# Kernel optimization log

Hardware: AMD Instinct MI355X
Metric: run time of the kernel (lower is better)

The kernel has to match this reference:

```python
import jax, jax.numpy as jnp
import numpy as np

IN_C = 256
KEY_C = 256
VAL_C = 256
HEADS = 8


def setup_inputs() -> dict:
    key = jax.random.key(0)
    ks = jax.random.split(key, 9)
    s = 0.02
    return {
        "x": jax.random.normal(ks[0], (4, 8192, IN_C), dtype=jnp.float32),
        "Wk": jax.random.normal(ks[1], (KEY_C, IN_C), dtype=jnp.float32) * s,
        "bk": jax.random.normal(ks[2], (KEY_C,), dtype=jnp.float32) * s,
        "Wq": jax.random.normal(ks[3], (KEY_C, IN_C), dtype=jnp.float32) * s,
        "bq": jax.random.normal(ks[4], (KEY_C,), dtype=jnp.float32) * s,
        "Wv": jax.random.normal(ks[5], (VAL_C, IN_C), dtype=jnp.float32) * s,
        "bv": jax.random.normal(ks[6], (VAL_C,), dtype=jnp.float32) * s,
        "Wr": jax.random.normal(ks[7], (IN_C, VAL_C), dtype=jnp.float32) * s,
        "br": jax.random.normal(ks[8], (IN_C,), dtype=jnp.float32) * s,
    }


def reference(x, Wk, bk, Wq, bq, Wv, bv, Wr, br):
    n, N, c = x.shape
    # Faithful to torch: reshape (NOT transpose) of (n, N, c) into (n, c, N)
    xi = x.reshape(n, c, N)
    # 1x1 convs == channel-mixing matmuls over the token axis
    K = jnp.einsum('oc,ncs->nos', Wk, xi) + bk[None, :, None]
    Q = jnp.einsum('oc,ncs->nos', Wq, xi) + bq[None, :, None]
    V = jnp.einsum('oc,ncs->nos', Wv, xi) + bv[None, :, None]
    dk = KEY_C // HEADS
    dv = VAL_C // HEADS
    Kh = K.reshape(n, HEADS, dk, N)
    Qh = Q.reshape(n, HEADS, dk, N)
    Vh = V.reshape(n, HEADS, dv, N)
    # keys: softmax over tokens (dim=2); queries: softmax over head key channels (dim=1)
    Kh = jax.nn.softmax(Kh, axis=3)
    Qh = jax.nn.softmax(Qh, axis=2)
    # context = K @ V^T : [n, H, dk, dv]
    ctx = jnp.einsum('nhks,nhvs->nhkv', Kh, Vh)
    # attended = context^T @ Q : [n, H, dv, N]
    att = jnp.einsum('nhkv,nhks->nhvs', ctx, Qh)
    agg = att.reshape(n, VAL_C, N)
    rep = jnp.einsum('ov,nvs->nos', Wr, agg) + br[None, :, None]
    out = rep + xi  # residual in (n, c, N) layout
    return jnp.transpose(out, (0, 2, 1))  # (n, N, c)
```

## Files before the change

### kernel.cpp

```cpp
#include <hip/hip_runtime.h>
#include <hip/hip_bf16.h>

#define NTOK 8192
#define NCH  256
#define TT   128
#define XTP  264
#define EK2  136

typedef unsigned short u16;
typedef __attribute__((ext_vector_type(8))) short bf16x8;
typedef __attribute__((ext_vector_type(4))) float f32x4;
typedef __attribute__((ext_vector_type(8))) unsigned short u16x8;
typedef __attribute__((ext_vector_type(4))) unsigned short u16x4;

__device__ __forceinline__ float b2f(u16 v){
  union { u16 u; __hip_bfloat16 h; } c; c.u = v; return __bfloat162float(c.h);
}
__device__ __forceinline__ u16 f2b(float f){
  union { __hip_bfloat16 h; u16 u; } c; c.h = __float2bfloat16(f); return c.u;
}
__device__ __forceinline__ f32x4 mfma16(bf16x8 a, bf16x8 b, f32x4 c){
  return __builtin_amdgcn_mfma_f32_16x16x32_bf16(a, b, c, 0, 0, 0);
}

__device__ __forceinline__ void stage_xtile(const float* __restrict__ xb,
                                            u16* scratch, u16* dst, int t)
{
  #pragma unroll
  for (int i = 0; i < 8; ++i) {
    int ch = i * 32 + (t >> 4);
    int tk = (t & 15) * 8;
    const float* p = xb + (size_t)ch * NTOK + tk;
    float4 v0 = *(const float4*)p;
    float4 v1 = *(const float4*)(p + 4);
    u16x8 pk;
    pk[0]=f2b(v0.x); pk[1]=f2b(v0.y); pk[2]=f2b(v0.z); pk[3]=f2b(v0.w);
    pk[4]=f2b(v1.x); pk[5]=f2b(v1.y); pk[6]=f2b(v1.z); pk[7]=f2b(v1.w);
    *(u16x8*)&scratch[ch * EK2 + tk] = pk;
  }
  __syncthreads();
  #pragma unroll
  for (int p2 = 0; p2 < 8; ++p2) {
    int idx = p2 * 512 + t;
    int tok = idx & 127;
    int ch = (idx >> 7) * 8;
    u16x8 o;
    #pragma unroll
    for (int j = 0; j < 8; ++j) o[j] = scratch[(ch + j) * EK2 + tok];
    *(u16x8*)&dst[tok * XTP + ch] = o;
  }
}

__global__ __launch_bounds__(256)
void k_prep(const float* __restrict__ Wk, const float* __restrict__ Wq,
            const float* __restrict__ Wv, const float* __restrict__ Wr,
            u16* __restrict__ wbf)
{
  const int t = threadIdx.x, bid = blockIdx.x;
  const int mat = bid >> 4;
  const float* src = (mat == 0) ? Wk : (mat == 1) ? Wq : (mat == 2) ? Wv : Wr;
  u16* dst = wbf + mat * 65536;
  const int base = (bid & 15) * 4096 + t * 16;
  #pragma unroll
  for (int i = 0; i < 4; ++i) {
    float4 v = *(const float4*)(src + base + i * 4);
    u16x4 pk; pk[0]=f2b(v.x); pk[1]=f2b(v.y); pk[2]=f2b(v.z); pk[3]=f2b(v.w);
    *(u16x4*)(dst + base + i * 4) = pk;
  }
}

__global__ __launch_bounds__(512, 2)
void k_ctx(const float* __restrict__ x, const u16* __restrict__ wbf,
           const float* __restrict__ bk, const float* __restrict__ bv,
           u16* __restrict__ ctxPart, float* __restrict__ denomPart)
{
  __shared__ u16 bufA[NCH * EK2];
  __shared__ u16 ekb[NCH * EK2];

  const int t = threadIdx.x;
  const int b = blockIdx.x >> 6, g = blockIdx.x & 63;
  const int w = t >> 6, lane = t & 63;
  const int l15 = lane & 15, quad = lane >> 4;
  const u16* Wkb = wbf;
  const u16* Wvb = wbf + 2 * 65536;

  stage_xtile(x + (size_t)b * NCH * NTOK + g * TT, ekb, bufA, t);
  __syncthreads();

  f32x4 acc[2][8];

  #pragma unroll
  for (int mi = 0; mi < 2; ++mi)
    #pragma unroll
    for (int nj = 0; nj < 8; ++nj) acc[mi][nj] = (f32x4)0.f;
  for (int k0 = 0; k0 < NCH; k0 += 32) {
    bf16x8 af[2], bx[8];
    #pragma unroll
    for (int mi = 0; mi < 2; ++mi)
      af[mi] = *(const bf16x8*)(Wkb + (size_t)(w * 32 + mi * 16 + l15) * NCH + k0 + quad * 8);
    #pragma unroll
    for (int nj = 0; nj < 8; ++nj)
      bx[nj] = *(const bf16x8*)&bufA[(nj * 16 + l15) * XTP + k0 + quad * 8];
    #pragma unroll
    for (int mi = 0; mi < 2; ++mi)
      #pragma unroll
      for (int nj = 0; nj < 8; ++nj) acc[mi][nj] = mfma16(af[mi], bx[nj], acc[mi][nj]);
  }
  #pragma unroll
  for (int mi = 0; mi < 2; ++mi) {
    float4 bb = *(const float4*)(bk + w * 32 + mi * 16 + quad * 4);
    #pragma unroll
    for (int nj = 0; nj < 8; ++nj) {
      int tok = nj * 16 + l15, chb = w * 32 + mi * 16 + quad * 4;
      ekb[(chb + 0) * EK2 + tok] = f2b(__expf(acc[mi][nj][0] + bb.x));
      ekb[(chb + 1) * EK2 + tok] = f2b(__expf(acc[mi][nj][1] + bb.y));
      ekb[(chb + 2) * EK2 + tok] = f2b(__expf(acc[mi][nj][2] + bb.z));
      ekb[(chb + 3) * EK2 + tok] = f2b(__expf(acc[mi][nj][3] + bb.w));
    }
  }

  #pragma unroll
  for (int mi = 0; mi < 2; ++mi)
    #pragma unroll
    for (int nj = 0; nj < 8; ++nj) acc[mi][nj] = (f32x4)0.f;
  for (int k0 = 0; k0 < NCH; k0 += 32) {
    bf16x8 af[2], bx[8];
    #pragma unroll
    for (int mi = 0; mi < 2; ++mi)
      af[mi] = *(const bf16x8*)(Wvb + (size_t)(w * 32 + mi * 16 + l15) * NCH + k0 + quad * 8);
    #pragma unroll
    for (int nj = 0; nj < 8; ++nj)
      bx[nj] = *(const bf16x8*)&bufA[(nj * 16 + l15) * XTP + k0 + quad * 8];
    #pragma unroll
    for (int mi = 0; mi < 2; ++mi)
      #pragma unroll
      for (int nj = 0; nj < 8; ++nj) acc[mi][nj] = mfma16(af[mi], bx[nj], acc[mi][nj]);
  }
  __syncthreads();
  #pragma unroll
  for (int mi = 0; mi < 2; ++mi) {
    float4 bb = *(const float4*)(bv + w * 32 + mi * 16 + quad * 4);
    #pragma unroll
    for (int nj = 0; nj < 8; ++nj) {
      int tok = nj * 16 + l15, chb = w * 32 + mi * 16 + quad * 4;
      bufA[(chb + 0) * EK2 + tok] = f2b(acc[mi][nj][0] + bb.x);
      bufA[(chb + 1) * EK2 + tok] = f2b(acc[mi][nj][1] + bb.y);
      bufA[(chb + 2) * EK2 + tok] = f2b(acc[mi][nj][2] + bb.z);
      bufA[(chb + 3) * EK2 + tok] = f2b(acc[mi][nj][3] + bb.w);
    }
  }
  __syncthreads();

  f32x4 cacc[2][2];
  #pragma unroll
  for (int mi = 0; mi < 2; ++mi)
    #pragma unroll
    for (int nj = 0; nj < 2; ++nj) cacc[mi][nj] = (f32x4)0.f;
  #pragma unroll
  for (int kc = 0; kc < 4; ++kc) {
    bf16x8 ae[2], bvv[2];
    #pragma unroll
    for (int mi = 0; mi < 2; ++mi)
      ae[mi] = *(const bf16x8*)&ekb[(w * 32 + mi * 16 + l15) * EK2 + kc * 32 + quad * 8];
    #pragma unroll
    for (int nj = 0; nj < 2; ++nj)
      bvv[nj] = *(const bf16x8*)&bufA[(w * 32 + nj * 16 + l15) * EK2 + kc * 32 + quad * 8];
    #pragma unroll
    for (int mi = 0; mi < 2; ++mi)
      #pragma unroll
      for (int nj = 0; nj < 2; ++nj)
        cacc[mi][nj] = mfma16(ae[mi], bvv[nj], cacc[mi][nj]);
  }
  float dsum = 0.f;
  if (t < 256) {
    #pragma unroll
    for (int s = 0; s < TT; s += 8) {
      u16x8 v = *(const u16x8*)&ekb[t * EK2 + s];
      #pragma unroll
      for (int j = 0; j < 8; ++j) dsum += b2f(v[j]);
    }
  }

  u16* cp = ctxPart + ((size_t)(b * 64 + g) << 13);
  #pragma unroll
  for (int mi = 0; mi < 2; ++mi)
    #pragma unroll
    for (int nj = 0; nj < 2; ++nj)
      #pragma unroll
      for (int r = 0; r < 4; ++r) {
        int e = ((w * 32 + mi * 16 + quad * 4 + r) << 5) + nj * 16 + l15;
        cp[e] = f2b(cacc[mi][nj][r]);
      }
  if (t < 256)
    denomPart[(size_t)(b * 64 + g) * 256 + t] = dsum;
}

__global__ __launch_bounds__(256)
void k_red(const u16* __restrict__ ctxPart, const float* __restrict__ denomPart,
           u16* __restrict__ ctxT, float* __restrict__ rdenomF)
{
  int i = blockIdx.x * 256 + threadIdx.x;
  if (i < 32768) {
    int b = i >> 13, e = i & 8191;
    const u16* p = ctxPart + ((size_t)(b * 64) << 13) + e;
    float s0 = 0.f, s1 = 0.f, s2 = 0.f, s3 = 0.f;
    #pragma unroll 4
    for (int g = 0; g < 64; g += 4) {
      s0 += b2f(p[(size_t)(g + 0) << 13]);
      s1 += b2f(p[(size_t)(g + 1) << 13]);
      s2 += b2f(p[(size_t)(g + 2) << 13]);
      s3 += b2f(p[(size_t)(g + 3) << 13]);
    }
    float s = (s0 + s1) + (s2 + s3);
    int hh = e >> 10, kk = (e >> 5) & 31, vch = e & 31;
    ctxT[(((b * 8 + hh) * 32 + vch) << 5) + kk] = f2b(s);
  } else if (i < 33792) {
    int j = i - 32768, b = j >> 8, ch = j & 255;
    const float* p = denomPart + (size_t)(b * 64) * 256 + ch;
    float s = 0.f;
    #pragma unroll 8
    for (int g = 0; g < 64; ++g) s += p[(size_t)g << 8];
    rdenomF[j] = 1.0f / s;
  }
}

__global__ __launch_bounds__(512, 2)
void k_out(const float* __restrict__ x, const u16* __restrict__ wbf,
           const float* __restrict__ bq, const float* __restrict__ br,
           const u16* __restrict__ ctxT, const float* __restrict__ rdenomF,
           float* __restrict__ out)
{
  __shared__ u16 xs[TT * XTP];
  __shared__ u16 qs[NCH * EK2];

  const int t = threadIdx.x;
  const int b = blockIdx.x >> 6, g = blockIdx.x & 63;
  const int w = t >> 6, lane = t & 63;
  const int l15 = lane & 15, quad = lane >> 4;
  const u16* Wqb = wbf + 65536;
  const u16* Wrb = wbf + 3 * 65536;

  stage_xtile(x + (size_t)b * NCH * NTOK + g * TT, qs, xs, t);
  __syncthreads();

  bf16x8 ac[2];
  #pragma unroll
  for (int mi = 0; mi < 2; ++mi)
    ac[mi] = *(const bf16x8*)(ctxT + (((size_t)(b * 8 + w) * 32 + mi * 16 + l15) << 5) + quad * 8);

  f32x4 acc[2][8];
  #pragma unroll
  for (int mi = 0; mi < 2; ++mi)
    #pragma unroll
    for (int nj = 0; nj < 8; ++nj) acc[mi][nj] = (f32x4)0.f;
  for (int k0 = 0; k0 < NCH; k0 += 32) {
    bf16x8 af[2], bx[8];
    #pragma unroll
    for (int mi = 0; mi < 2; ++mi)
      af[mi] = *(const bf16x8*)(Wqb + (size_t)(w * 32 + mi * 16 + l15) * NCH + k0 + quad * 8);
    #pragma unroll
    for (int nj = 0; nj < 8; ++nj)
      bx[nj] = *(const bf16x8*)&xs[(nj * 16 + l15) * XTP + k0 + quad * 8];
    #pragma unroll
    for (int mi = 0; mi < 2; ++mi)
      #pragma unroll
      for (int nj = 0; nj < 8; ++nj) acc[mi][nj] = mfma16(af[mi], bx[nj], acc[mi][nj]);
  }
  #pragma unroll
  for (int mi = 0; mi < 2; ++mi) {
    float4 bb = *(const float4*)(bq + w * 32 + mi * 16 + quad * 4);
    #pragma unroll
    for (int nj = 0; nj < 8; ++nj) {
      acc[mi][nj][0] = __expf(acc[mi][nj][0] + bb.x);
      acc[mi][nj][1] = __expf(acc[mi][nj][1] + bb.y);
      acc[mi][nj][2] = __expf(acc[mi][nj][2] + bb.z);
      acc[mi][nj][3] = __expf(acc[mi][nj][3] + bb.w);
    }
  }
  float inv[8];
  #pragma unroll
  for (int nj = 0; nj < 8; ++nj) {
    float s = 0.f;
    #pragma unroll
    for (int mi = 0; mi < 2; ++mi)
      #pragma unroll
      for (int r = 0; r < 4; ++r) s += acc[mi][nj][r];
    s += __shfl_xor(s, 16);
    s += __shfl_xor(s, 32);
    inv[nj] = 1.0f / s;
  }
  #pragma unroll
  for (int mi = 0; mi < 2; ++mi) {
    float4 rd = *(const float4*)(rdenomF + b * 256 + w * 32 + mi * 16 + quad * 4);
    #pragma unroll
    for (int nj = 0; nj < 8; ++nj) {
      u16x4 pk;
      pk[0] = f2b(acc[mi][nj][0] * inv[nj] * rd.x);
      pk[1] = f2b(acc[mi][nj][1] * inv[nj] * rd.y);
      pk[2] = f2b(acc[mi][nj][2] * inv[nj] * rd.z);
      pk[3] = f2b(acc[mi][nj][3] * inv[nj] * rd.w);
      *(u16x4*)&qs[(nj * 16 + l15) * XTP + w * 32 + mi * 16 + quad * 4] = pk;
    }
  }
  __syncthreads();

  f32x4 aacc[2][8];
  {
    #pragma unroll
    for (int nj = 0; nj < 8; ++nj) {
      bf16x8 bqf = *(const bf16x8*)&qs[(nj * 16 + l15) * XTP + w * 32 + quad * 8];
      #pragma unroll
      for (int mi = 0; mi < 2; ++mi)
        aacc[mi][nj] = mfma16(ac[mi], bqf, (f32x4)0.f);
    }
  }
  #pragma unroll
  for (int mi = 0; mi < 2; ++mi)
    #pragma unroll
    for (int nj = 0; nj < 8; ++nj) {
      u16x4 pk;
      pk[0] = f2b(aacc[mi][nj][0]);
      pk[1] = f2b(aacc[mi][nj][1]);
      pk[2] = f2b(aacc[mi][nj][2]);
      pk[3] = f2b(aacc[mi][nj][3]);
      *(u16x4*)&qs[(nj * 16 + l15) * XTP + w * 32 + mi * 16 + quad * 4] = pk;
    }
  __syncthreads();

  #pragma unroll
  for (int mi = 0; mi < 2; ++mi)
    #pragma unroll
    for (int nj = 0; nj < 8; ++nj) acc[mi][nj] = (f32x4)0.f;
  for (int k0 = 0; k0 < NCH; k0 += 32) {
    bf16x8 af[2], bx[8];
    #pragma unroll
    for (int mi = 0; mi < 2; ++mi)
      af[mi] = *(const bf16x8*)(Wrb + (size_t)(w * 32 + mi * 16 + l15) * NCH + k0 + quad * 8);
    #pragma unroll
    for (int nj = 0; nj < 8; ++nj)
      bx[nj] = *(const bf16x8*)&qs[(nj * 16 + l15) * XTP + k0 + quad * 8];
    #pragma unroll
    for (int mi = 0; mi < 2; ++mi)
      #pragma unroll
      for (int nj = 0; nj < 8; ++nj) acc[mi][nj] = mfma16(af[mi], bx[nj], acc[mi][nj]);
  }
  #pragma unroll
  for (int mi = 0; mi < 2; ++mi) {
    float4 bb = *(const float4*)(br + w * 32 + mi * 16 + quad * 4);
    #pragma unroll
    for (int nj = 0; nj < 8; ++nj) {
      int tok = nj * 16 + l15;
      u16x4 rx = *(const u16x4*)&xs[tok * XTP + w * 32 + mi * 16 + quad * 4];
      float4 o;
      o.x = acc[mi][nj][0] + bb.x + b2f(rx[0]);
      o.y = acc[mi][nj][1] + bb.y + b2f(rx[1]);
      o.z = acc[mi][nj][2] + bb.z + b2f(rx[2]);
      o.w = acc[mi][nj][3] + bb.w + b2f(rx[3]);
      *(float4*)(out + (((size_t)(b * NTOK + g * TT + tok)) << 8) + w * 32 + mi * 16 + quad * 4) = o;
    }
  }
}

extern "C" void kernel_launch(void* const* d_in, const int* in_sizes, int n_in,
                              void* d_out, int out_size, void* d_ws, size_t ws_size,
                              hipStream_t stream) {
  const float* x  = (const float*)d_in[0];
  const float* Wk = (const float*)d_in[1];
  const float* bk = (const float*)d_in[2];
  const float* Wq = (const float*)d_in[3];
  const float* bq = (const float*)d_in[4];
  const float* Wv = (const float*)d_in[5];
  const float* bv = (const float*)d_in[6];
  const float* Wr = (const float*)d_in[7];
  const float* br = (const float*)d_in[8];
  float* out = (float*)d_out;

  char* wsb = (char*)d_ws;
  u16*   ctxPart   = (u16*)wsb;
  float* denomPart = (float*)(wsb + 4194304);
  u16*   ctxT      = (u16*)(wsb + 4456448);
  float* rdenomF   = (float*)(wsb + 4521984);
  u16*   wbf       = (u16*)(wsb + 4526080);

  hipLaunchKernelGGL(k_prep, dim3(64), dim3(256), 0, stream,
                     Wk, Wq, Wv, Wr, wbf);
  hipLaunchKernelGGL(k_ctx, dim3(256), dim3(512), 0, stream,
                     x, wbf, bk, bv, ctxPart, denomPart);
  hipLaunchKernelGGL(k_red, dim3(132), dim3(256), 0, stream,
                     ctxPart, denomPart, ctxT, rdenomF);
  hipLaunchKernelGGL(k_out, dim3(256), dim3(512), 0, stream,
                     x, wbf, bq, br, ctxT, rdenomF, out);
}
```

Before: 132.6 us.

## Fuse ctx, reduce and output kernels into one persistent kernel with grid barriers

```diff
diff --git a/kernel.cpp b/kernel.cpp
--- a/kernel.cpp
+++ b/kernel.cpp
@@ -6,6 +6,7 @@
 #define TT   128
 #define XTP  264
 #define EK2  136
+#define NBLK 256
 
 typedef unsigned short u16;
 typedef __attribute__((ext_vector_type(8))) short bf16x8;
@@ -21,6 +22,18 @@
 }
 __device__ __forceinline__ f32x4 mfma16(bf16x8 a, bf16x8 b, f32x4 c){
   return __builtin_amdgcn_mfma_f32_16x16x32_bf16(a, b, c, 0, 0, 0);
+}
+
+__device__ __forceinline__ void grid_sync(unsigned* cnt, int t) {
+  __syncthreads();
+  if (t == 0) {
+    __threadfence();
+    __hip_atomic_fetch_add(cnt, 1u, __ATOMIC_ACQ_REL, __HIP_MEMORY_SCOPE_AGENT);
+    while (__hip_atomic_load(cnt, __ATOMIC_ACQUIRE, __HIP_MEMORY_SCOPE_AGENT) < NBLK)
+      __builtin_amdgcn_s_sleep(1);
+    __threadfence();
+  }
+  __syncthreads();
 }
 
 __device__ __forceinline__ void stage_xtile(const float* __restrict__ xb,
@@ -54,9 +67,10 @@
 __global__ __launch_bounds__(256)
 void k_prep(const float* __restrict__ Wk, const float* __restrict__ Wq,
             const float* __restrict__ Wv, const float* __restrict__ Wr,
-            u16* __restrict__ wbf)
+            u16* __restrict__ wbf, unsigned* __restrict__ cnt)
 {
   const int t = threadIdx.x, bid = blockIdx.x;
+  if (bid == 0 && t == 0) { cnt[0] = 0u; cnt[1] = 0u; }
   const int mat = bid >> 4;
   const float* src = (mat == 0) ? Wk : (mat == 1) ? Wq : (mat == 2) ? Wv : Wr;
   u16* dst = wbf + mat * 65536;
@@ -70,9 +84,12 @@
 }
 
 __global__ __launch_bounds__(512, 2)
-void k_ctx(const float* __restrict__ x, const u16* __restrict__ wbf,
-           const float* __restrict__ bk, const float* __restrict__ bv,
-           u16* __restrict__ ctxPart, float* __restrict__ denomPart)
+void k_main(const float* __restrict__ x, const u16* __restrict__ wbf,
+            const float* __restrict__ bk, const float* __restrict__ bv,
+            const float* __restrict__ bq, const float* __restrict__ br,
+            u16* __restrict__ ctxPart, float* __restrict__ denomPart,
+            u16* __restrict__ ctxT, float* __restrict__ rdenomF,
+            float* __restrict__ out, unsigned* __restrict__ cnt)
 {
   __shared__ u16 bufA[NCH * EK2];
   __shared__ u16 ekb[NCH * EK2];
@@ -82,165 +99,157 @@
   const int w = t >> 6, lane = t & 63;
   const int l15 = lane & 15, quad = lane >> 4;
   const u16* Wkb = wbf;
+  const u16* Wqb = wbf + 65536;
   const u16* Wvb = wbf + 2 * 65536;
-
-  stage_xtile(x + (size_t)b * NCH * NTOK + g * TT, ekb, bufA, t);
-  __syncthreads();
-
-  f32x4 acc[2][8];
-
-  #pragma unroll
-  for (int mi = 0; mi < 2; ++mi)
-    #pragma unroll
-    for (int nj = 0; nj < 8; ++nj) acc[mi][nj] = (f32x4)0.f;
-  for (int k0 = 0; k0 < NCH; k0 += 32) {
-    bf16x8 af[2], bx[8];
-    #pragma unroll
-    for (int mi = 0; mi < 2; ++mi)
-      af[mi] = *(const bf16x8*)(Wkb + (size_t)(w * 32 + mi * 16 + l15) * NCH + k0 + quad * 8);
-    #pragma unroll
-    for (int nj = 0; nj < 8; ++nj)
-      bx[nj] = *(const bf16x8*)&bufA[(nj * 16 + l15) * XTP + k0 + quad * 8];
-    #pragma unroll
-    for (int mi = 0; mi < 2; ++mi)
-      #pragma unroll
-      for (int nj = 0; nj < 8; ++nj) acc[mi][nj] = mfma16(af[mi], bx[nj], acc[mi][nj]);
-  }
-  #pragma unroll
-  for (int mi = 0; mi < 2; ++mi) {
-    float4 bb = *(const float4*)(bk + w * 32 + mi * 16 + quad * 4);
-    #pragma unroll
-    for (int nj = 0; nj < 8; ++nj) {
-      int tok = nj * 16 + l15, chb = w * 32 + mi * 16 + quad * 4;
-      ekb[(chb + 0) * EK2 + tok] = f2b(__expf(acc[mi][nj][0] + bb.x));
-      ekb[(chb + 1) * EK2 + tok] = f2b(__expf(acc[mi][nj][1] + bb.y));
-      ekb[(chb + 2) * EK2 + tok] = f2b(__expf(acc[mi][nj][2] + bb.z));
-      ekb[(chb + 3) * EK2 + tok] = f2b(__expf(acc[mi][nj][3] + bb.w));
-    }
-  }
-
-  #pragma unroll
-  for (int mi = 0; mi < 2; ++mi)
-    #pragma unroll
-    for (int nj = 0; nj < 8; ++nj) acc[mi][nj] = (f32x4)0.f;
-  for (int k0 = 0; k0 < NCH; k0 += 32) {
-    bf16x8 af[2], bx[8];
-    #pragma unroll
-    for (int mi = 0; mi < 2; ++mi)
-      af[mi] = *(const bf16x8*)(Wvb + (size_t)(w * 32 + mi * 16 + l15) * NCH + k0 + quad * 8);
-    #pragma unroll
-    for (int nj = 0; nj < 8; ++nj)
-      bx[nj] = *(const bf16x8*)&bufA[(nj * 16 + l15) * XTP + k0 + quad * 8];
-    #pragma unroll
-    for (int mi = 0; mi < 2; ++mi)
-      #pragma unroll
-      for (int nj = 0; nj < 8; ++nj) acc[mi][nj] = mfma16(af[mi], bx[nj], acc[mi][nj]);
-  }
-  __syncthreads();
-  #pragma unroll
-  for (int mi = 0; mi < 2; ++mi) {
-    float4 bb = *(const float4*)(bv + w * 32 + mi * 16 + quad * 4);
-    #pragma unroll
-    for (int nj = 0; nj < 8; ++nj) {
-      int tok = nj * 16 + l15, chb = w * 32 + mi * 16 + quad * 4;
-      bufA[(chb + 0) * EK2 + tok] = f2b(acc[mi][nj][0] + bb.x);
-      bufA[(chb + 1) * EK2 + tok] = f2b(acc[mi][nj][1] + bb.y);
-      bufA[(chb + 2) * EK2 + tok] = f2b(acc[mi][nj][2] + bb.z);
-      bufA[(chb + 3) * EK2 + tok] = f2b(acc[mi][nj][3] + bb.w);
-    }
-  }
-  __syncthreads();
-
-  f32x4 cacc[2][2];
-  #pragma unroll
-  for (int mi = 0; mi < 2; ++mi)
-    #pragma unroll
-    for (int nj = 0; nj < 2; ++nj) cacc[mi][nj] = (f32x4)0.f;
-  #pragma unroll
-  for (int kc = 0; kc < 4; ++kc) {
-    bf16x8 ae[2], bvv[2];
-    #pragma unroll
-    for (int mi = 0; mi < 2; ++mi)
-      ae[mi] = *(const bf16x8*)&ekb[(w * 32 + mi * 16 + l15) * EK2 + kc * 32 + quad * 8];
-    #pragma unroll
-    for (int nj = 0; nj < 2; ++nj)
-      bvv[nj] = *(const bf16x8*)&bufA[(w * 32 + nj * 16 + l15) * EK2 + kc * 32 + quad * 8];
-    #pragma unroll
-    for (int mi = 0; mi < 2; ++mi)
+  const u16* Wrb = wbf + 3 * 65536;
+  const float* xb = x + (size_t)b * NCH * NTOK + g * TT;
+
+  stage_xtile(xb, ekb, bufA, t);
+  __syncthreads();
+
+  {
+    f32x4 acc[2][8];
+
+    #pragma unroll
+    for (int mi = 0; mi < 2; ++mi)
+      #pragma unroll
+      for (int nj = 0; nj < 8; ++nj) acc[mi][nj] = (f32x4)0.f;
+    for (int k0 = 0; k0 < NCH; k0 += 32) {
+      bf16x8 af[2], bx[8];
+      #pragma unroll
+      for (int mi = 0; mi < 2; ++mi)
+        af[mi] = *(const bf16x8*)(Wkb + (size_t)(w * 32 + mi * 16 + l15) * NCH + k0 + quad * 8);
+      #pragma unroll
+      for (int nj = 0; nj < 8; ++nj)
+        bx[nj] = *(const bf16x8*)&bufA[(nj * 16 + l15) * XTP + k0 + quad * 8];
+      #pragma unroll
+      for (int mi = 0; mi < 2; ++mi)
+        #pragma unroll
+        for (int nj = 0; nj < 8; ++nj) acc[mi][nj] = mfma16(af[mi], bx[nj], acc[mi][nj]);
+    }
+    #pragma unroll
+    for (int mi = 0; mi < 2; ++mi) {
+      float4 bb = *(const float4*)(bk + w * 32 + mi * 16 + quad * 4);
+      #pragma unroll
+      for (int nj = 0; nj < 8; ++nj) {
+        int tok = nj * 16 + l15, chb = w * 32 + mi * 16 + quad * 4;
+        ekb[(chb + 0) * EK2 + tok] = f2b(__expf(acc[mi][nj][0] + bb.x));
+        ekb[(chb + 1) * EK2 + tok] = f2b(__expf(acc[mi][nj][1] + bb.y));
+        ekb[(chb + 2) * EK2 + tok] = f2b(__expf(acc[mi][nj][2] + bb.z));
+        ekb[(chb + 3) * EK2 + tok] = f2b(__expf(acc[mi][nj][3] + bb.w));
+      }
+    }
+
+    #pragma unroll
+    for (int mi = 0; mi < 2; ++mi)
+      #pragma unroll
+      for (int nj = 0; nj < 8; ++nj) acc[mi][nj] = (f32x4)0.f;
+    for (int k0 = 0; k0 < NCH; k0 += 32) {
+      bf16x8 af[2], bx[8];
+      #pragma unroll
+      for (int mi = 0; mi < 2; ++mi)
+        af[mi] = *(const bf16x8*)(Wvb + (size_t)(w * 32 + mi * 16 + l15) * NCH + k0 + quad * 8);
+      #pragma unroll
+      for (int nj = 0; nj < 8; ++nj)
+        bx[nj] = *(const bf16x8*)&bufA[(nj * 16 + l15) * XTP + k0 + quad * 8];
+      #pragma unroll
+      for (int mi = 0; mi < 2; ++mi)
+        #pragma unroll
+        for (int nj = 0; nj < 8; ++nj) acc[mi][nj] = mfma16(af[mi], bx[nj], acc[mi][nj]);
+    }
+    __syncthreads();
+    #pragma unroll
+    for (int mi = 0; mi < 2; ++mi) {
+      float4 bb = *(const float4*)(bv + w * 32 + mi * 16 + quad * 4);
+      #pragma unroll
+      for (int nj = 0; nj < 8; ++nj) {
+        int tok = nj * 16 + l15, chb = w * 32 + mi * 16 + quad * 4;
+        bufA[(chb + 0) * EK2 + tok] = f2b(acc[mi][nj][0] + bb.x);
+        bufA[(chb + 1) * EK2 + tok] = f2b(acc[mi][nj][1] + bb.y);
+        bufA[(chb + 2) * EK2 + tok] = f2b(acc[mi][nj][2] + bb.z);
+        bufA[(chb + 3) * EK2 + tok] = f2b(acc[mi][nj][3] + bb.w);
+      }
+    }
+    __syncthreads();
+
+    f32x4 cacc[2][2];
+    #pragma unroll
+    for (int mi = 0; mi < 2; ++mi)
+      #pragma unroll
+      for (int nj = 0; nj < 2; ++nj) cacc[mi][nj] = (f32x4)0.f;
+    #pragma unroll
+    for (int kc = 0; kc < 4; ++kc) {
+      bf16x8 ae[2], bvv[2];
+      #pragma unroll
+      for (int mi = 0; mi < 2; ++mi)
+        ae[mi] = *(const bf16x8*)&ekb[(w * 32 + mi * 16 + l15) * EK2 + kc * 32 + quad * 8];
       #pragma unroll
       for (int nj = 0; nj < 2; ++nj)
-        cacc[mi][nj] = mfma16(ae[mi], bvv[nj], cacc[mi][nj]);
-  }
-  float dsum = 0.f;
-  if (t < 256) {
-    #pragma unroll
-    for (int s = 0; s < TT; s += 8) {
-      u16x8 v = *(const u16x8*)&ekb[t * EK2 + s];
-      #pragma unroll
-      for (int j = 0; j < 8; ++j) dsum += b2f(v[j]);
-    }
-  }
-
-  u16* cp = ctxPart + ((size_t)(b * 64 + g) << 13);
-  #pragma unroll
-  for (int mi = 0; mi < 2; ++mi)
-    #pragma unroll
-    for (int nj = 0; nj < 2; ++nj)
-      #pragma unroll
-      for (int r = 0; r < 4; ++r) {
-        int e = ((w * 32 + mi * 16 + quad * 4 + r) << 5) + nj * 16 + l15;
-        cp[e] = f2b(cacc[mi][nj][r]);
+        bvv[nj] = *(const bf16x8*)&bufA[(w * 32 + nj * 16 + l15) * EK2 + kc * 32 + quad * 8];
+      #pragma unroll
+      for (int mi = 0; mi < 2; ++mi)
+        #pragma unroll
+        for (int nj = 0; nj < 2; ++nj)
+          cacc[mi][nj] = mfma16(ae[mi], bvv[nj], cacc[mi][nj]);
+    }
+    float dsum = 0.f;
+    if (t < 256) {
+      #pragma unroll
+      for (int s = 0; s < TT; s += 8) {
+        u16x8 v = *(const u16x8*)&ekb[t * EK2 + s];
+        #pragma unroll
+        for (int j = 0; j < 8; ++j) dsum += b2f(v[j]);
       }
-  if (t < 256)
-    denomPart[(size_t)(b * 64 + g) * 256 + t] = dsum;
-}
-
-__global__ __launch_bounds__(256)
-void k_red(const u16* __restrict__ ctxPart, const float* __restrict__ denomPart,
-           u16* __restrict__ ctxT, float* __restrict__ rdenomF)
-{
-  int i = blockIdx.x * 256 + threadIdx.x;
-  if (i < 32768) {
-    int b = i >> 13, e = i & 8191;
-    const u16* p = ctxPart + ((size_t)(b * 64) << 13) + e;
-    float s0 = 0.f, s1 = 0.f, s2 = 0.f, s3 = 0.f;
-    #pragma unroll 4
-    for (int g = 0; g < 64; g += 4) {
-      s0 += b2f(p[(size_t)(g + 0) << 13]);
-      s1 += b2f(p[(size_t)(g + 1) << 13]);
-      s2 += b2f(p[(size_t)(g + 2) << 13]);
-      s3 += b2f(p[(size_t)(g + 3) << 13]);
-    }
-    float s = (s0 + s1) + (s2 + s3);
-    int hh = e >> 10, kk = (e >> 5) & 31, vch = e & 31;
-    ctxT[(((b * 8 + hh) * 32 + vch) << 5) + kk] = f2b(s);
-  } else if (i < 33792) {
-    int j = i - 32768, b = j >> 8, ch = j & 255;
-    const float* p = denomPart + (size_t)(b * 64) * 256 + ch;
-    float s = 0.f;
-    #pragma unroll 8
-    for (int g = 0; g < 64; ++g) s += p[(size_t)g << 8];
-    rdenomF[j] = 1.0f / s;
-  }
-}
-
-__global__ __launch_bounds__(512, 2)
-void k_out(const float* __restrict__ x, const u16* __restrict__ wbf,
-           const float* __restrict__ bq, const float* __restrict__ br,
-           const u16* __restrict__ ctxT, const float* __restrict__ rdenomF,
-           float* __restrict__ out)
-{
-  __shared__ u16 xs[TT * XTP];
-  __shared__ u16 qs[NCH * EK2];
-
-  const int t = threadIdx.x;
-  const int b = blockIdx.x >> 6, g = blockIdx.x & 63;
-  const int w = t >> 6, lane = t & 63;
-  const int l15 = lane & 15, quad = lane >> 4;
-  const u16* Wqb = wbf + 65536;
-  const u16* Wrb = wbf + 3 * 65536;
-
-  stage_xtile(x + (size_t)b * NCH * NTOK + g * TT, qs, xs, t);
+    }
+
+    u16* cp = ctxPart + ((size_t)(b * 64 + g) << 13);
+    #pragma unroll
+    for (int mi = 0; mi < 2; ++mi)
+      #pragma unroll
+      for (int nj = 0; nj < 2; ++nj)
+        #pragma unroll
+        for (int r = 0; r < 4; ++r) {
+          int e = ((w * 32 + mi * 16 + quad * 4 + r) << 5) + nj * 16 + l15;
+          cp[e] = f2b(cacc[mi][nj][r]);
+        }
+    if (t < 256)
+      denomPart[(size_t)(b * 64 + g) * 256 + t] = dsum;
+  }
+
+  grid_sync(&cnt[0], t);
+
+  {
+    const int gid = blockIdx.x * 512 + t;
+    if (gid < 32768) {
+      const int b2 = gid >> 13, e = gid & 8191;
+      const u16* p = ctxPart + (((size_t)b2 * 64) << 13) + e;
+      float s0 = 0.f, s1 = 0.f, s2 = 0.f, s3 = 0.f;
+      #pragma unroll 4
+      for (int g2 = 0; g2 < 64; g2 += 4) {
+        s0 += b2f(p[(size_t)(g2 + 0) << 13]);
+        s1 += b2f(p[(size_t)(g2 + 1) << 13]);
+        s2 += b2f(p[(size_t)(g2 + 2) << 13]);
+        s3 += b2f(p[(size_t)(g2 + 3) << 13]);
+      }
+      float s = (s0 + s1) + (s2 + s3);
+      int hh = e >> 10, kk = (e >> 5) & 31, vch = e & 31;
+      ctxT[(((b2 * 8 + hh) * 32 + vch) << 5) + kk] = f2b(s);
+    } else if (gid < 33792) {
+      int j = gid - 32768, b2 = j >> 8, ch = j & 255;
+      const float* p = denomPart + (size_t)(b2 * 64) * 256 + ch;
+      float s = 0.f;
+      #pragma unroll 8
+      for (int g2 = 0; g2 < 64; ++g2) s += p[(size_t)g2 << 8];
+      rdenomF[j] = 1.0f / s;
+    }
+  }
+
+  grid_sync(&cnt[1], t);
+
+  u16* xs = bufA;
+  u16* qs = ekb;
+
+  stage_xtile(xb, qs, xs, t);
   __syncthreads();
 
   bf16x8 ac[2];
@@ -376,18 +385,16 @@
   float* out = (float*)d_out;
 
   char* wsb = (char*)d_ws;
-  u16*   ctxPart   = (u16*)wsb;
-  float* denomPart = (float*)(wsb + 4194304);
-  u16*   ctxT      = (u16*)(wsb + 4456448);
-  float* rdenomF   = (float*)(wsb + 4521984);
-  u16*   wbf       = (u16*)(wsb + 4526080);
+  u16*      ctxPart   = (u16*)wsb;
+  float*    denomPart = (float*)(wsb + 4194304);
+  u16*      ctxT      = (u16*)(wsb + 4456448);
+  float*    rdenomF   = (float*)(wsb + 4521984);
+  u16*      wbf       = (u16*)(wsb + 4526080);
+  unsigned* cnt       = (unsigned*)(wsb + 5050368);
 
   hipLaunchKernelGGL(k_prep, dim3(64), dim3(256), 0, stream,
-                     Wk, Wq, Wv, Wr, wbf);
-  hipLaunchKernelGGL(k_ctx, dim3(256), dim3(512), 0, stream,
-                     x, wbf, bk, bv, ctxPart, denomPart);
-  hipLaunchKernelGGL(k_red, dim3(132), dim3(256), 0, stream,
-                     ctxPart, denomPart, ctxT, rdenomF);
-  hipLaunchKernelGGL(k_out, dim3(256), dim3(512), 0, stream,
-                     x, wbf, bq, br, ctxT, rdenomF, out);
-}
+                     Wk, Wq, Wv, Wr, wbf, cnt);
+  hipLaunchKernelGGL(k_main, dim3(NBLK), dim3(512), 0, stream,
+                     x, wbf, bk, bv, bq, br,
+                     ctxPart, denomPart, ctxT, rdenomF, out, cnt);
+}
```

Result: slower. 185.4 us (+39.7%).

## Fuse partial context reduction into output kernel, dropping separate reduce launch

Applied to the files above, without the earlier changes.

```diff
diff --git a/kernel.cpp b/kernel.cpp
--- a/kernel.cpp
+++ b/kernel.cpp
@@ -195,43 +195,16 @@
     denomPart[(size_t)(b * 64 + g) * 256 + t] = dsum;
 }
 
-__global__ __launch_bounds__(256)
-void k_red(const u16* __restrict__ ctxPart, const float* __restrict__ denomPart,
-           u16* __restrict__ ctxT, float* __restrict__ rdenomF)
-{
-  int i = blockIdx.x * 256 + threadIdx.x;
-  if (i < 32768) {
-    int b = i >> 13, e = i & 8191;
-    const u16* p = ctxPart + ((size_t)(b * 64) << 13) + e;
-    float s0 = 0.f, s1 = 0.f, s2 = 0.f, s3 = 0.f;
-    #pragma unroll 4
-    for (int g = 0; g < 64; g += 4) {
-      s0 += b2f(p[(size_t)(g + 0) << 13]);
-      s1 += b2f(p[(size_t)(g + 1) << 13]);
-      s2 += b2f(p[(size_t)(g + 2) << 13]);
-      s3 += b2f(p[(size_t)(g + 3) << 13]);
-    }
-    float s = (s0 + s1) + (s2 + s3);
-    int hh = e >> 10, kk = (e >> 5) & 31, vch = e & 31;
-    ctxT[(((b * 8 + hh) * 32 + vch) << 5) + kk] = f2b(s);
-  } else if (i < 33792) {
-    int j = i - 32768, b = j >> 8, ch = j & 255;
-    const float* p = denomPart + (size_t)(b * 64) * 256 + ch;
-    float s = 0.f;
-    #pragma unroll 8
-    for (int g = 0; g < 64; ++g) s += p[(size_t)g << 8];
-    rdenomF[j] = 1.0f / s;
-  }
-}
-
 __global__ __launch_bounds__(512, 2)
 void k_out(const float* __restrict__ x, const u16* __restrict__ wbf,
            const float* __restrict__ bq, const float* __restrict__ br,
-           const u16* __restrict__ ctxT, const float* __restrict__ rdenomF,
+           const u16* __restrict__ ctxPart, const float* __restrict__ denomPart,
            float* __restrict__ out)
 {
   __shared__ u16 xs[TT * XTP];
   __shared__ u16 qs[NCH * EK2];
+  __shared__ u16 ctxbuf[8192];
+  __shared__ float rdnbuf[256];
 
   const int t = threadIdx.x;
   const int b = blockIdx.x >> 6, g = blockIdx.x & 63;
@@ -243,10 +216,33 @@
   stage_xtile(x + (size_t)b * NCH * NTOK + g * TT, qs, xs, t);
   __syncthreads();
 
-  bf16x8 ac[2];
-  #pragma unroll
-  for (int mi = 0; mi < 2; ++mi)
-    ac[mi] = *(const bf16x8*)(ctxT + (((size_t)(b * 8 + w) * 32 + mi * 16 + l15) << 5) + quad * 8);
+  {
+    #pragma unroll
+    for (int half = 0; half < 2; ++half) {
+      const int e0 = half * 4096 + t * 8;
+      const u16* p = ctxPart + ((size_t)(b * 64) << 13) + e0;
+      float s[8];
+      #pragma unroll
+      for (int j = 0; j < 8; ++j) s[j] = 0.f;
+      #pragma unroll 4
+      for (int g2 = 0; g2 < 64; ++g2) {
+        u16x8 v = *(const u16x8*)(p + ((size_t)g2 << 13));
+        #pragma unroll
+        for (int j = 0; j < 8; ++j) s[j] += b2f(v[j]);
+      }
+      const int hh = e0 >> 10, kkl = (e0 >> 5) & 31, vch0 = e0 & 31;
+      #pragma unroll
+      for (int j = 0; j < 8; ++j)
+        ctxbuf[((hh * 32 + vch0 + j) << 5) + kkl] = f2b(s[j]);
+    }
+    if (t < 256) {
+      const float* p = denomPart + (size_t)(b * 64) * 256 + t;
+      float s = 0.f;
+      #pragma unroll 8
+      for (int g2 = 0; g2 < 64; ++g2) s += p[(size_t)g2 << 8];
+      rdnbuf[t] = 1.0f / s;
+    }
+  }
 
   f32x4 acc[2][8];
   #pragma unroll
@@ -291,18 +287,32 @@
   }
   #pragma unroll
   for (int mi = 0; mi < 2; ++mi) {
-    float4 rd = *(const float4*)(rdenomF + b * 256 + w * 32 + mi * 16 + quad * 4);
     #pragma unroll
     for (int nj = 0; nj < 8; ++nj) {
       u16x4 pk;
-      pk[0] = f2b(acc[mi][nj][0] * inv[nj] * rd.x);
-      pk[1] = f2b(acc[mi][nj][1] * inv[nj] * rd.y);
-      pk[2] = f2b(acc[mi][nj][2] * inv[nj] * rd.z);
-      pk[3] = f2b(acc[mi][nj][3] * inv[nj] * rd.w);
+      pk[0] = f2b(acc[mi][nj][0] * inv[nj]);
+      pk[1] = f2b(acc[mi][nj][1] * inv[nj]);
+      pk[2] = f2b(acc[mi][nj][2] * inv[nj]);
+      pk[3] = f2b(acc[mi][nj][3] * inv[nj]);
       *(u16x4*)&qs[(nj * 16 + l15) * XTP + w * 32 + mi * 16 + quad * 4] = pk;
     }
   }
   __syncthreads();
+
+  bf16x8 ac[2];
+  {
+    float rd[8];
+    #pragma unroll
+    for (int j = 0; j < 8; ++j) rd[j] = rdnbuf[w * 32 + quad * 8 + j];
+    #pragma unroll
+    for (int mi = 0; mi < 2; ++mi) {
+      #pragma unroll
+      for (int j = 0; j < 8; ++j) {
+        u16 c = ctxbuf[((w * 32 + mi * 16 + l15) << 5) + quad * 8 + j];
+        ac[mi][j] = (short)f2b(b2f(c) * rd[j]);
+      }
+    }
+  }
 
   f32x4 aacc[2][8];
   {
@@ -378,16 +388,12 @@
   char* wsb = (char*)d_ws;
   u16*   ctxPart   = (u16*)wsb;
   float* denomPart = (float*)(wsb + 4194304);
-  u16*   ctxT      = (u16*)(wsb + 4456448);
-  float* rdenomF   = (float*)(wsb + 4521984);
-  u16*   wbf       = (u16*)(wsb + 4526080);
+  u16*   wbf       = (u16*)(wsb + 4456448);
 
   hipLaunchKernelGGL(k_prep, dim3(64), dim3(256), 0, stream,
                      Wk, Wq, Wv, Wr, wbf);
   hipLaunchKernelGGL(k_ctx, dim3(256), dim3(512), 0, stream,
                      x, wbf, bk, bv, ctxPart, denomPart);
-  hipLaunchKernelGGL(k_red, dim3(132), dim3(256), 0, stream,
-                     ctxPart, denomPart, ctxT, rdenomF);
   hipLaunchKernelGGL(k_out, dim3(256), dim3(512), 0, stream,
-                     x, wbf, bq, br, ctxT, rdenomF, out);
-}
+                     x, wbf, bq, br, ctxPart, denomPart, out);
+}
```

Result: slower. 144.1 us (+8.6%).
